# Performance work log

Hardware: AMD Instinct MI355X
Metric: run time of the kernel (lower is better)

## Reference

```python
import jax, jax.numpy as jnp
import numpy as np

D_MODEL = 2048
NUM_HEADS = 16
D_K = D_MODEL // NUM_HEADS
SEQ = 2048
BATCH = 2
THETA = 10000.0


def setup_inputs() -> dict:
    key = jax.random.key(0)
    ks = jax.random.split(key, 5)
    s = 1.0 / np.sqrt(D_MODEL)
    return {
        "x": jax.random.normal(ks[0], (BATCH, SEQ, D_MODEL), jnp.float32),
        "wq": jax.random.normal(ks[1], (D_MODEL, D_MODEL), jnp.float32) * s,
        "wk": jax.random.normal(ks[2], (D_MODEL, D_MODEL), jnp.float32) * s,
        "wv": jax.random.normal(ks[3], (D_MODEL, D_MODEL), jnp.float32) * s,
        "wo": jax.random.normal(ks[4], (D_MODEL, D_MODEL), jnp.float32) * s,
    }


def _rope_tables(seq_len, d_k, theta, dtype):
    pos = jnp.arange(seq_len, dtype=dtype)[:, None]            # [S,1]
    inv = theta ** (-(jnp.arange(0, d_k, 2, dtype=dtype) / d_k))  # [d_k/2]
    ang = pos * inv                                            # [S, d_k/2]
    sin = jnp.repeat(jnp.sin(ang), 2, axis=1)                  # [S, d_k] interleaved
    cos = jnp.repeat(jnp.cos(ang), 2, axis=1)
    return sin, cos


def _apply_rope(x, sin, cos):
    # x: [..., S, d_k]; interleaved-pair rotation
    xp = x.reshape(x.shape[:-1] + (x.shape[-1] // 2, 2))
    swapped = jnp.stack((-xp[..., 1], xp[..., 0]), axis=-1).reshape(x.shape)
    return x * cos + swapped * sin


def reference(x, wq, wk, wv, wo):
    B, S, D = x.shape
    H, dk = NUM_HEADS, D_K
    # projections: weights are (H*dk, D); q/k/v -> [B,H,S,dk]
    q = jnp.einsum("bsd,hkd->bhsk", x, wq.reshape(H, dk, D))
    k = jnp.einsum("bsd,hkd->bhsk", x, wk.reshape(H, dk, D))
    v = jnp.einsum("bsd,hkd->bhsk", x, wv.reshape(H, dk, D))
    sin, cos = _rope_tables(S, dk, THETA, x.dtype)
    q = _apply_rope(q, sin, cos)
    k = _apply_rope(k, sin, cos)
    scores = jnp.einsum("bhqk,bhsk->bhqs", q, k) / jnp.sqrt(jnp.asarray(dk, x.dtype))
    causal = jnp.triu(jnp.ones((S, S), dtype=bool), k=1)
    scores = jnp.where(causal, -jnp.inf, scores)
    attn = jax.nn.softmax(scores, axis=-1)
    out = jnp.einsum("bhqs,bhsv->bqhv", attn, v).reshape(B, S, H * dk)
    return jnp.einsum("bsf,df->bsd", out, wo)
```

## Files before the change

### kernel.cpp

```cpp
#include <hip/hip_runtime.h>
#include <hip/hip_bf16.h>

#define B_  2
#define S_  2048
#define D_  2048
#define H_  16
#define DK_ 128
#define M_  (B_*S_)

typedef unsigned short u16;
typedef short bf16x8 __attribute__((ext_vector_type(8)));
typedef float f32x4  __attribute__((ext_vector_type(4)));

#define NEG_BIG (-1.0e30f)

__device__ __forceinline__ u16 f2bf(float f){
    unsigned int u = __float_as_uint(f);
    unsigned int r = (u + 0x7fffu + ((u >> 16) & 1u)) >> 16;
    return (u16)r;
}

__device__ __forceinline__ uint4 cvt8(const float* p){
    float4 a = *(const float4*)p;
    float4 b = *(const float4*)(p + 4);
    uint4 r;
    r.x = ((unsigned int)f2bf(a.y) << 16) | (unsigned int)f2bf(a.x);
    r.y = ((unsigned int)f2bf(a.w) << 16) | (unsigned int)f2bf(a.z);
    r.z = ((unsigned int)f2bf(b.y) << 16) | (unsigned int)f2bf(b.x);
    r.w = ((unsigned int)f2bf(b.w) << 16) | (unsigned int)f2bf(b.z);
    return r;
}

__device__ __forceinline__ void unpack8(const uint4 v, float* f){
    f[0]=__uint_as_float(v.x<<16); f[1]=__uint_as_float(v.x&0xffff0000u);
    f[2]=__uint_as_float(v.y<<16); f[3]=__uint_as_float(v.y&0xffff0000u);
    f[4]=__uint_as_float(v.z<<16); f[5]=__uint_as_float(v.z&0xffff0000u);
    f[6]=__uint_as_float(v.w<<16); f[7]=__uint_as_float(v.w&0xffff0000u);
}

__device__ __forceinline__ void async16(const void* g, void* l){
    __builtin_amdgcn_global_load_lds(
        (const __attribute__((address_space(1))) void*)g,
        (__attribute__((address_space(3))) void*)l, 16, 0, 0);
}

__global__ __launch_bounds__(256) void cvt_all(
    const float* __restrict__ x,  const float* __restrict__ wq, const float* __restrict__ wk,
    const float* __restrict__ wv, const float* __restrict__ wo,
    u16* __restrict__ xb, u16* __restrict__ wqb, u16* __restrict__ wkb,
    u16* __restrict__ wvb, u16* __restrict__ wob)
{
    int c = blockIdx.x*256 + threadIdx.x;
    const float* src; u16* dst; int lc;
    if      (c < 1048576){ src = x;  dst = xb;  lc = c; }
    else if (c < 1572864){ src = wq; dst = wqb; lc = c - 1048576; }
    else if (c < 2097152){ src = wk; dst = wkb; lc = c - 1572864; }
    else if (c < 2621440){ src = wv; dst = wvb; lc = c - 2097152; }
    else                 { src = wo; dst = wob; lc = c - 2621440; }
    *(uint4*)&dst[(size_t)lc*8] = cvt8(&src[(size_t)lc*8]);
}

template<int MODE>
__global__ __launch_bounds__(512, 2) void gemm256(
    const u16* __restrict__ A, const u16* __restrict__ W0, const u16* __restrict__ W1,
    void* __restrict__ C0, void* __restrict__ C1)
{
    __shared__ __align__(16) u16 ring[4][2][8192];

    const int tid  = threadIdx.x;
    const int lane = tid & 63;
    const int w    = tid >> 6;
    const int quad = lane >> 4;
    const int l15  = lane & 15;
    const int wM   = w & 1;
    const int wN   = w >> 1;
    const int blockN = blockIdx.x * 256;
    const int blockM = blockIdx.y * 256;

    const u16* Wm; void* Cm;
    if (MODE == 0){ Wm = blockIdx.z ? W1 : W0; Cm = blockIdx.z ? (void*)C1 : (void*)C0; }
    else          { Wm = W0; Cm = C0; }

    const int cswz = quad ^ ((l15 >> 1) & 3);

    f32x4 acc[32];
    #pragma unroll
    for (int i = 0; i < 32; ++i) acc[i] = (f32x4){0.f,0.f,0.f,0.f};

    auto stage = [&](int t){
        const int k0 = t * 32;
        u16* la = (u16*)&ring[t & 3][0][0];
        u16* lb = (u16*)&ring[t & 3][1][0];
        #pragma unroll
        for (int it = 0; it < 2; ++it){
            int cc  = it*512 + tid;
            int row = cc >> 2;
            int g   = (cc & 3) ^ ((cc >> 3) & 3);
            int kb  = k0 + g*8;
            const u16* ga;
            if (MODE == 1){
                int rg = blockM + row;
                int b = rg >> 11, s2 = rg & 2047;
                int h = kb >> 7,  kk = kb & 127;
                ga = &A[(((size_t)(b*H_ + h))*S_ + s2)*DK_ + kk];
            } else {
                ga = &A[(size_t)(blockM + row)*2048 + kb];
            }
            async16(ga, la + cc*8);
            async16(&Wm[(size_t)(blockN + row)*2048 + kb], lb + cc*8);
        }
    };

    stage(0); stage(1); stage(2);
    asm volatile("s_waitcnt vmcnt(8)" ::: "memory");
    __builtin_amdgcn_s_barrier();
    __builtin_amdgcn_sched_barrier(0);

    for (int t = 0; t < 64; ++t){
        const u16* la = (const u16*)&ring[t & 3][0][0];
        const u16* lb = (const u16*)&ring[t & 3][1][0];

        if (t <= 60) stage(t + 3);

        bf16x8 bfv[4], af[4];
        #pragma unroll
        for (int ni = 0; ni < 4; ++ni)
            bfv[ni] = *(const bf16x8*)&lb[(wN*64 + ni*16 + l15)*32 + cswz*8];
        #pragma unroll
        for (int mi = 0; mi < 4; ++mi)
            af[mi]  = *(const bf16x8*)&la[(wM*128 + mi*16 + l15)*32 + cswz*8];

        __builtin_amdgcn_s_setprio(1);
        #pragma unroll
        for (int mi = 0; mi < 4; ++mi)
            #pragma unroll
            for (int ni = 0; ni < 4; ++ni)
                acc[mi*4+ni] = __builtin_amdgcn_mfma_f32_16x16x32_bf16(
                                   af[mi], bfv[ni], acc[mi*4+ni], 0, 0, 0);
        __builtin_amdgcn_s_setprio(0);

        #pragma unroll
        for (int mi = 0; mi < 4; ++mi)
            af[mi]  = *(const bf16x8*)&la[(wM*128 + 64 + mi*16 + l15)*32 + cswz*8];

        __builtin_amdgcn_s_setprio(1);
        #pragma unroll
        for (int mi = 0; mi < 4; ++mi)
            #pragma unroll
            for (int ni = 0; ni < 4; ++ni)
                acc[16 + mi*4+ni] = __builtin_amdgcn_mfma_f32_16x16x32_bf16(
                                   af[mi], bfv[ni], acc[16 + mi*4+ni], 0, 0, 0);
        __builtin_amdgcn_s_setprio(0);

        if (t <= 60)      { asm volatile("s_waitcnt vmcnt(8)" ::: "memory"); }
        else if (t == 61) { asm volatile("s_waitcnt vmcnt(4)" ::: "memory"); }
        else if (t == 62) { asm volatile("s_waitcnt vmcnt(0)" ::: "memory"); }
        __builtin_amdgcn_s_barrier();
        __builtin_amdgcn_sched_barrier(0);
    }

    #pragma unroll
    for (int hf = 0; hf < 2; ++hf){
        #pragma unroll
        for (int mi = 0; mi < 4; ++mi){
            #pragma unroll
            for (int ni = 0; ni < 4; ++ni){
                #pragma unroll
                for (int r = 0; r < 4; ++r){
                    float v = acc[hf*16 + mi*4+ni][r];
                    int row = blockM + wM*128 + hf*64 + mi*16 + quad*4 + r;
                    int col = blockN + wN*64 + ni*16 + l15;
                    if (MODE == 0){
                        int b = row >> 11, s2 = row & 2047;
                        int h = col >> 7,  kk = col & 127;
                        ((u16*)Cm)[(((size_t)(b*H_ + h))*S_ + s2)*DK_ + kk] = f2bf(v);
                    } else if (MODE == 2){
                        int h = row >> 7,  kk = row & 127;
                        int b = col >> 11, s2 = col & 2047;
                        ((u16*)Cm)[(((size_t)(b*H_ + h))*DK_ + kk)*S_ + s2] = f2bf(v);
                    } else {
                        ((float*)Cm)[(size_t)row*2048 + col] = v;
                    }
                }
            }
        }
    }
}

template<int MODE>
__global__ __launch_bounds__(256) void gemm_bt(
    const void* __restrict__ Av,
    const float* __restrict__ W0, const float* __restrict__ W1,
    void* __restrict__ C0, void* __restrict__ C1)
{
    __shared__ u16 As[128*40];
    __shared__ u16 Bs[128*40];

    const int tid  = threadIdx.x;
    const int lane = tid & 63;
    const int w    = tid >> 6;
    const int quad = lane >> 4;
    const int l15  = lane & 15;
    const int blockN = blockIdx.x * 128;
    const int blockM = blockIdx.y * 128;

    const float* Wm; void* Cm;
    if (MODE == 0){ Wm = blockIdx.z ? W1 : W0; Cm = blockIdx.z ? (void*)C1 : (void*)C0; }
    else          { Wm = W0; Cm = C0; }

    const int waveM = (w & 1) * 64;
    const int waveN = (w >> 1) * 64;

    f32x4 acc[16];
    #pragma unroll
    for (int i = 0; i < 16; ++i) acc[i] = (f32x4){0.f,0.f,0.f,0.f};

    for (int k0 = 0; k0 < 2048; k0 += 32){
        __syncthreads();
        #pragma unroll
        for (int it = 0; it < 2; ++it){
            int cc  = tid + it*256;
            int row = cc >> 2;
            int ch  = cc & 3;
            int kb  = k0 + ch*8;
            uint4 va;
            if (MODE == 1){
                int g = blockM + row;
                int b = g >> 11, s2 = g & 2047;
                int h = kb >> 7, kk = kb & 127;
                va = *(const uint4*)&((const u16*)Av)[(((size_t)(b*H_ + h))*S_ + s2)*DK_ + kk];
            } else {
                va = cvt8(&((const float*)Av)[(size_t)(blockM+row)*2048 + kb]);
            }
            uint4 vb = cvt8(&Wm[(size_t)(blockN+row)*2048 + kb]);
            *(uint4*)&As[row*40 + ch*8] = va;
            *(uint4*)&Bs[row*40 + ch*8] = vb;
        }
        __syncthreads();

        bf16x8 af[4], bfv[4];
        #pragma unroll
        for (int mi = 0; mi < 4; ++mi)
            af[mi]  = *(const bf16x8*)&As[(waveM + mi*16 + l15)*40 + quad*8];
        #pragma unroll
        for (int ni = 0; ni < 4; ++ni)
            bfv[ni] = *(const bf16x8*)&Bs[(waveN + ni*16 + l15)*40 + quad*8];
        #pragma unroll
        for (int mi = 0; mi < 4; ++mi)
            #pragma unroll
            for (int ni = 0; ni < 4; ++ni)
                acc[mi*4+ni] = __builtin_amdgcn_mfma_f32_16x16x32_bf16(
                                   af[mi], bfv[ni], acc[mi*4+ni], 0, 0, 0);
    }

    #pragma unroll
    for (int mi = 0; mi < 4; ++mi){
        #pragma unroll
        for (int ni = 0; ni < 4; ++ni){
            #pragma unroll
            for (int r = 0; r < 4; ++r){
                float v = acc[mi*4+ni][r];
                int row = blockM + waveM + mi*16 + quad*4 + r;
                int col = blockN + waveN + ni*16 + l15;
                if (MODE == 0){
                    int b = row >> 11, s2 = row & 2047;
                    int h = col >> 7,  kk = col & 127;
                    ((u16*)Cm)[(((size_t)(b*H_ + h))*S_ + s2)*DK_ + kk] = f2bf(v);
                } else if (MODE == 2){
                    int h = row >> 7,  kk = row & 127;
                    int b = col >> 11, s2 = col & 2047;
                    ((u16*)Cm)[(((size_t)(b*H_ + h))*DK_ + kk)*S_ + s2] = f2bf(v);
                } else {
                    ((float*)Cm)[(size_t)row*2048 + col] = v;
                }
            }
        }
    }
}

__global__ __launch_bounds__(256) void rope_kernel(u16* __restrict__ Q, u16* __restrict__ K)
{
    u16* T = blockIdx.y ? K : Q;
    const float osc = blockIdx.y ? 1.0f : 0.12751743f;
    int t  = blockIdx.x * 256 + threadIdx.x;
    int i0 = (t & 15) * 4;
    int s  = (t >> 4) & 2047;
    size_t base = ((size_t)(t >> 4)) * 128 + (size_t)i0 * 2;
    uint4 v = *(const uint4*)&T[base];
    float f[8]; unpack8(v, f);
    const float nl2t = -13.287712379549449f / 64.0f;
    float sf = (float)s;
    unsigned int out[4];
    #pragma unroll
    for (int p = 0; p < 4; ++p){
        float inv = exp2f((float)(i0 + p) * nl2t);
        float ang = sf * inv;
        float sn, cn;
        sincosf(ang, &sn, &cn);
        float e0 = f[2*p], e1 = f[2*p+1];
        float r0 = (e0*cn - e1*sn) * osc;
        float r1 = (e1*cn + e0*sn) * osc;
        out[p] = ((unsigned int)f2bf(r1) << 16) | (unsigned int)f2bf(r0);
    }
    uint4 ov; ov.x = out[0]; ov.y = out[1]; ov.z = out[2]; ov.w = out[3];
    *(uint4*)&T[base] = ov;
}

__global__ __launch_bounds__(256, 4) void attn_mfma(
    const u16* Q, const u16* __restrict__ K,
    const u16* __restrict__ VT, u16* O)
{
    __shared__ __align__(16) u16 Ks[64*128];
    __shared__ __align__(16) u16 Vs[128*64];
    __shared__ __align__(16) u16 Ps[4][16*64];

    const int tid  = threadIdx.x;
    const int bh   = blockIdx.x;
    const int qb   = (int)gridDim.y - 1 - (int)blockIdx.y;
    const int w    = tid >> 6;
    const int lane = tid & 63;
    const int quad = lane >> 4;
    const int l15  = lane & 15;
    const int sw   = l15 & 7;
    const size_t qkb = (size_t)bh * S_ * DK_;

    const int qw = qb*64 + w*16;

    bf16x8 aq[4];
    {
        const u16* qp = &Q[qkb + (size_t)(qw + l15)*128 + quad*8];
        #pragma unroll
        for (int kt = 0; kt < 4; ++kt)
            aq[kt] = *(const bf16x8*)(qp + kt*32);
    }

    f32x4 oa[8];
    #pragma unroll
    for (int vt = 0; vt < 8; ++vt) oa[vt] = (f32x4){0.f,0.f,0.f,0.f};
    float m_i = NEG_BIG, l_i = 0.f;

    const int nkb = qb + 1;
    for (int kb = 0; kb < nkb; ++kb){
        __syncthreads();
        #pragma unroll
        for (int it = 0; it < 4; ++it){
            int cc  = tid + it*256;
            int row = cc >> 4, cl = cc & 15;
            async16(&K[qkb + (size_t)(kb*64 + row)*128 + (size_t)((cl ^ (row & 7))*8)],
                    &Ks[cc*8]);
        }
        #pragma unroll
        for (int it = 0; it < 4; ++it){
            int cc  = tid + it*256;
            int row = cc >> 3, cl = cc & 7;
            async16(&VT[qkb + (size_t)row*S_ + (size_t)(kb*64 + (cl ^ (row & 7))*8)],
                    &Vs[cc*8]);
        }
        __syncthreads();

        if (kb*64 > qw + 15) continue;

        f32x4 s[4];
        __builtin_amdgcn_s_setprio(1);
        #pragma unroll
        for (int nt = 0; nt < 4; ++nt){
            f32x4 a = (f32x4){0.f,0.f,0.f,0.f};
            #pragma unroll
            for (int kt = 0; kt < 4; ++kt){
                bf16x8 ak = *(const bf16x8*)&Ks[(nt*16 + l15)*128 + ((kt*4 + quad) ^ sw)*8];
                a = __builtin_amdgcn_mfma_f32_16x16x32_bf16(ak, aq[kt], a, 0,0,0);
            }
            s[nt] = a;
        }
        __builtin_amdgcn_s_setprio(0);

        if (kb*64 + 63 > qw){
            int qg = qw + l15;
            #pragma unroll
            for (int nt = 0; nt < 4; ++nt)
                #pragma unroll
                for (int rr = 0; rr < 4; ++rr){
                    int jg = kb*64 + nt*16 + quad*4 + rr;
                    if (jg > qg) s[nt][rr] = NEG_BIG;
                }
        }

        float mx = s[0][0];
        #pragma unroll
        for (int nt = 0; nt < 4; ++nt)
            #pragma unroll
            for (int rr = 0; rr < 4; ++rr) mx = fmaxf(mx, s[nt][rr]);
        mx = fmaxf(mx, __shfl_xor(mx, 16, 64));
        mx = fmaxf(mx, __shfl_xor(mx, 32, 64));

        if (!__all((mx - m_i) <= 8.0f)){
            float mn = fmaxf(m_i, mx);
            float al = exp2f(m_i - mn);
            m_i = mn;
            l_i *= al;
            float al4[4];
            #pragma unroll
            for (int rr = 0; rr < 4; ++rr)
                al4[rr] = __shfl(al, (lane & 48) | (quad*4 + rr), 64);
            #pragma unroll
            for (int vt = 0; vt < 8; ++vt)
                #pragma unroll
                for (int rr = 0; rr < 4; ++rr) oa[vt][rr] *= al4[rr];
        }

        float ps = 0.f;
        #pragma unroll
        for (int nt = 0; nt < 4; ++nt)
            #pragma unroll
            for (int rr = 0; rr < 4; ++rr){
                float p = exp2f(s[nt][rr] - m_i);
                s[nt][rr] = p; ps += p;
            }
        ps += __shfl_xor(ps, 16, 64);
        ps += __shfl_xor(ps, 32, 64);
        l_i += ps;

        u16* pw = Ps[w];
        #pragma unroll
        for (int nt = 0; nt < 4; ++nt){
            uint2 pk;
            asm("v_cvt_pk_bf16_f32 %0, %1, %2" : "=v"(pk.x) : "v"(s[nt][0]), "v"(s[nt][1]));
            asm("v_cvt_pk_bf16_f32 %0, %1, %2" : "=v"(pk.y) : "v"(s[nt][2]), "v"(s[nt][3]));
            int c = (nt*2 + (quad >> 1)) ^ sw;
            *(uint2*)&pw[l15*64 + c*8 + (quad & 1)*4] = pk;
        }

        bf16x8 pa[2];
        #pragma unroll
        for (int kt = 0; kt < 2; ++kt)
            pa[kt] = *(const bf16x8*)&pw[l15*64 + ((kt*4 + quad) ^ sw)*8];

        __builtin_amdgcn_s_setprio(1);
        #pragma unroll
        for (int vt = 0; vt < 8; ++vt){
            #pragma unroll
            for (int kt = 0; kt < 2; ++kt){
                bf16x8 bv = *(const bf16x8*)&Vs[(vt*16 + l15)*64 + ((kt*4 + quad) ^ sw)*8];
                oa[vt] = __builtin_amdgcn_mfma_f32_16x16x32_bf16(pa[kt], bv, oa[vt], 0,0,0);
            }
        }
        __builtin_amdgcn_s_setprio(0);
    }

    #pragma unroll
    for (int rr = 0; rr < 4; ++rr){
        float lv = __shfl(l_i, (lane & 48) | (quad*4 + rr), 64);
        float inv = 1.f / lv;
        int qg = qw + quad*4 + rr;
        #pragma unroll
        for (int vt = 0; vt < 8; ++vt)
            O[qkb + (size_t)qg*128 + vt*16 + l15] = f2bf(oa[vt][rr] * inv);
    }
}

extern "C" void kernel_launch(void* const* d_in, const int* in_sizes, int n_in,
                              void* d_out, int out_size, void* d_ws, size_t ws_size,
                              hipStream_t stream)
{
    const float* x  = (const float*)d_in[0];
    const float* wq = (const float*)d_in[1];
    const float* wk = (const float*)d_in[2];
    const float* wv = (const float*)d_in[3];
    const float* wo = (const float*)d_in[4];
    float* out = (float*)d_out;

    const size_t NT = (size_t)B_ * H_ * S_ * DK_;
    const size_t NW = (size_t)D_ * D_;

    if (ws_size >= (size_t)50331648){
        u16* Qw  = (u16*)d_ws;
        u16* Kw  = Qw + NT;
        u16* wvb = Qw + 2*NT;
        u16* wob = wvb + NW;
        u16* xb  = (u16*)d_out;
        u16* wqb = xb + NT;
        u16* wkb = wqb + NW;
        u16* VT  = xb + NT;
        u16* Ow  = Qw;

        cvt_all<<<dim3(12288), 256, 0, stream>>>(x, wq, wk, wv, wo,
                                                 xb, wqb, wkb, wvb, wob);
        gemm256<0><<<dim3(8, 16, 2), 512, 0, stream>>>(xb, wqb, wkb, Qw, Kw);
        gemm256<2><<<dim3(16, 8, 1), 512, 0, stream>>>(wvb, xb, nullptr, VT, nullptr);
        rope_kernel<<<dim3(4096, 2), 256, 0, stream>>>(Qw, Kw);
        attn_mfma<<<dim3(32, 32), 256, 0, stream>>>(Qw, Kw, VT, Ow);
        gemm256<1><<<dim3(8, 16, 1), 512, 0, stream>>>(Ow, wob, nullptr, out, nullptr);
    } else {
        u16* Qw  = (u16*)d_ws;
        u16* Vtd = (u16*)d_out;
        u16* Kw  = (u16*)d_out + NT;
        u16* Ow  = Qw;
        gemm_bt<0><<<dim3(16, 32, 2), 256, 0, stream>>>(x, wq, wk, Qw, Kw);
        gemm_bt<2><<<dim3(32, 16, 1), 256, 0, stream>>>(wv, x, nullptr, Vtd, nullptr);
        rope_kernel<<<dim3(4096, 2), 256, 0, stream>>>(Qw, Kw);
        attn_mfma<<<dim3(32, 32), 256, 0, stream>>>(Qw, Kw, Vtd, Ow);
        gemm_bt<1><<<dim3(16, 32, 1), 256, 0, stream>>>(Ow, wo, nullptr, out, nullptr);
    }
}
```

Baseline: 396.1 us.

## Process two 16-row query tiles per warp in attention kernel

```diff
diff --git a/kernel.cpp b/kernel.cpp
--- a/kernel.cpp
+++ b/kernel.cpp
@@ -306,13 +306,13 @@
     *(uint4*)&T[base] = ov;
 }
 
-__global__ __launch_bounds__(256, 4) void attn_mfma(
+__global__ __launch_bounds__(256, 3) void attn_mfma(
     const u16* Q, const u16* __restrict__ K,
     const u16* __restrict__ VT, u16* O)
 {
     __shared__ __align__(16) u16 Ks[64*128];
     __shared__ __align__(16) u16 Vs[128*64];
-    __shared__ __align__(16) u16 Ps[4][16*64];
+    __shared__ __align__(16) u16 Ps[4][32*64];
 
     const int tid  = threadIdx.x;
     const int bh   = blockIdx.x;
@@ -324,22 +324,27 @@
     const int sw   = l15 & 7;
     const size_t qkb = (size_t)bh * S_ * DK_;
 
-    const int qw = qb*64 + w*16;
-
-    bf16x8 aq[4];
-    {
-        const u16* qp = &Q[qkb + (size_t)(qw + l15)*128 + quad*8];
+    const int qw = qb*128 + w*32;
+
+    bf16x8 aq[2][4];
+    #pragma unroll
+    for (int mt = 0; mt < 2; ++mt){
+        const u16* qp = &Q[qkb + (size_t)(qw + mt*16 + l15)*128 + quad*8];
         #pragma unroll
         for (int kt = 0; kt < 4; ++kt)
-            aq[kt] = *(const bf16x8*)(qp + kt*32);
-    }
-
-    f32x4 oa[8];
-    #pragma unroll
-    for (int vt = 0; vt < 8; ++vt) oa[vt] = (f32x4){0.f,0.f,0.f,0.f};
-    float m_i = NEG_BIG, l_i = 0.f;
-
-    const int nkb = qb + 1;
+            aq[mt][kt] = *(const bf16x8*)(qp + kt*32);
+    }
+
+    f32x4 oa[2][8];
+    float m_i[2], l_i[2];
+    #pragma unroll
+    for (int mt = 0; mt < 2; ++mt){
+        #pragma unroll
+        for (int vt = 0; vt < 8; ++vt) oa[mt][vt] = (f32x4){0.f,0.f,0.f,0.f};
+        m_i[mt] = NEG_BIG; l_i[mt] = 0.f;
+    }
+
+    const int nkb = 2*qb + 2;
     for (int kb = 0; kb < nkb; ++kb){
         __syncthreads();
         #pragma unroll
@@ -358,103 +363,126 @@
         }
         __syncthreads();
 
-        if (kb*64 > qw + 15) continue;
-
-        f32x4 s[4];
+        if (kb*64 > qw + 31) continue;
+
+        f32x4 s[2][4];
         __builtin_amdgcn_s_setprio(1);
         #pragma unroll
         for (int nt = 0; nt < 4; ++nt){
-            f32x4 a = (f32x4){0.f,0.f,0.f,0.f};
-            #pragma unroll
-            for (int kt = 0; kt < 4; ++kt){
-                bf16x8 ak = *(const bf16x8*)&Ks[(nt*16 + l15)*128 + ((kt*4 + quad) ^ sw)*8];
-                a = __builtin_amdgcn_mfma_f32_16x16x32_bf16(ak, aq[kt], a, 0,0,0);
-            }
-            s[nt] = a;
+            bf16x8 ak[4];
+            #pragma unroll
+            for (int kt = 0; kt < 4; ++kt)
+                ak[kt] = *(const bf16x8*)&Ks[(nt*16 + l15)*128 + ((kt*4 + quad) ^ sw)*8];
+            #pragma unroll
+            for (int mt = 0; mt < 2; ++mt){
+                f32x4 a = (f32x4){0.f,0.f,0.f,0.f};
+                #pragma unroll
+                for (int kt = 0; kt < 4; ++kt)
+                    a = __builtin_amdgcn_mfma_f32_16x16x32_bf16(ak[kt], aq[mt][kt], a, 0,0,0);
+                s[mt][nt] = a;
+            }
         }
         __builtin_amdgcn_s_setprio(0);
 
         if (kb*64 + 63 > qw){
-            int qg = qw + l15;
+            #pragma unroll
+            for (int mt = 0; mt < 2; ++mt){
+                int qg = qw + mt*16 + l15;
+                #pragma unroll
+                for (int nt = 0; nt < 4; ++nt)
+                    #pragma unroll
+                    for (int rr = 0; rr < 4; ++rr){
+                        int jg = kb*64 + nt*16 + quad*4 + rr;
+                        if (jg > qg) s[mt][nt][rr] = NEG_BIG;
+                    }
+            }
+        }
+
+        #pragma unroll
+        for (int mt = 0; mt < 2; ++mt){
+            float mx = s[mt][0][0];
             #pragma unroll
             for (int nt = 0; nt < 4; ++nt)
                 #pragma unroll
+                for (int rr = 0; rr < 4; ++rr) mx = fmaxf(mx, s[mt][nt][rr]);
+            mx = fmaxf(mx, __shfl_xor(mx, 16, 64));
+            mx = fmaxf(mx, __shfl_xor(mx, 32, 64));
+
+            if (!__all((mx - m_i[mt]) <= 8.0f)){
+                float mn = fmaxf(m_i[mt], mx);
+                float al = exp2f(m_i[mt] - mn);
+                m_i[mt] = mn;
+                l_i[mt] *= al;
+                float al4[4];
+                #pragma unroll
+                for (int rr = 0; rr < 4; ++rr)
+                    al4[rr] = __shfl(al, (lane & 48) | (quad*4 + rr), 64);
+                #pragma unroll
+                for (int vt = 0; vt < 8; ++vt)
+                    #pragma unroll
+                    for (int rr = 0; rr < 4; ++rr) oa[mt][vt][rr] *= al4[rr];
+            }
+
+            float ps = 0.f;
+            #pragma unroll
+            for (int nt = 0; nt < 4; ++nt)
+                #pragma unroll
                 for (int rr = 0; rr < 4; ++rr){
-                    int jg = kb*64 + nt*16 + quad*4 + rr;
-                    if (jg > qg) s[nt][rr] = NEG_BIG;
+                    float p = exp2f(s[mt][nt][rr] - m_i[mt]);
+                    s[mt][nt][rr] = p; ps += p;
                 }
-        }
-
-        float mx = s[0][0];
-        #pragma unroll
-        for (int nt = 0; nt < 4; ++nt)
-            #pragma unroll
-            for (int rr = 0; rr < 4; ++rr) mx = fmaxf(mx, s[nt][rr]);
-        mx = fmaxf(mx, __shfl_xor(mx, 16, 64));
-        mx = fmaxf(mx, __shfl_xor(mx, 32, 64));
-
-        if (!__all((mx - m_i) <= 8.0f)){
-            float mn = fmaxf(m_i, mx);
-            float al = exp2f(m_i - mn);
-            m_i = mn;
-            l_i *= al;
-            float al4[4];
-            #pragma unroll
-            for (int rr = 0; rr < 4; ++rr)
-                al4[rr] = __shfl(al, (lane & 48) | (quad*4 + rr), 64);
+            ps += __shfl_xor(ps, 16, 64);
+            ps += __shfl_xor(ps, 32, 64);
+            l_i[mt] += ps;
+        }
+
+        u16* pw = Ps[w];
+        #pragma unroll
+        for (int mt = 0; mt < 2; ++mt)
+          #pragma unroll
+          for (int nt = 0; nt < 4; ++nt){
+              uint2 pk;
+              asm("v_cvt_pk_bf16_f32 %0, %1, %2" : "=v"(pk.x) : "v"(s[mt][nt][0]), "v"(s[mt][nt][1]));
+              asm("v_cvt_pk_bf16_f32 %0, %1, %2" : "=v"(pk.y) : "v"(s[mt][nt][2]), "v"(s[mt][nt][3]));
+              int c = (nt*2 + (quad >> 1)) ^ sw;
+              *(uint2*)&pw[(mt*16 + l15)*64 + c*8 + (quad & 1)*4] = pk;
+          }
+
+        bf16x8 pa[2][2];
+        #pragma unroll
+        for (int mt = 0; mt < 2; ++mt)
+          #pragma unroll
+          for (int kt = 0; kt < 2; ++kt)
+            pa[mt][kt] = *(const bf16x8*)&pw[(mt*16 + l15)*64 + ((kt*4 + quad) ^ sw)*8];
+
+        __builtin_amdgcn_s_setprio(1);
+        #pragma unroll
+        for (int vt = 0; vt < 8; ++vt){
+            bf16x8 bv[2];
+            #pragma unroll
+            for (int kt = 0; kt < 2; ++kt)
+                bv[kt] = *(const bf16x8*)&Vs[(vt*16 + l15)*64 + ((kt*4 + quad) ^ sw)*8];
+            #pragma unroll
+            for (int mt = 0; mt < 2; ++mt)
+              #pragma unroll
+              for (int kt = 0; kt < 2; ++kt)
+                oa[mt][vt] = __builtin_amdgcn_mfma_f32_16x16x32_bf16(
+                                 pa[mt][kt], bv[kt], oa[mt][vt], 0,0,0);
+        }
+        __builtin_amdgcn_s_setprio(0);
+    }
+
+    #pragma unroll
+    for (int mt = 0; mt < 2; ++mt){
+        #pragma unroll
+        for (int rr = 0; rr < 4; ++rr){
+            float lv = __shfl(l_i[mt], (lane & 48) | (quad*4 + rr), 64);
+            float inv = 1.f / lv;
+            int qg = qw + mt*16 + quad*4 + rr;
             #pragma unroll
             for (int vt = 0; vt < 8; ++vt)
-                #pragma unroll
-                for (int rr = 0; rr < 4; ++rr) oa[vt][rr] *= al4[rr];
-        }
-
-        float ps = 0.f;
-        #pragma unroll
-        for (int nt = 0; nt < 4; ++nt)
-            #pragma unroll
-            for (int rr = 0; rr < 4; ++rr){
-                float p = exp2f(s[nt][rr] - m_i);
-                s[nt][rr] = p; ps += p;
-            }
-        ps += __shfl_xor(ps, 16, 64);
-        ps += __shfl_xor(ps, 32, 64);
-        l_i += ps;
-
-        u16* pw = Ps[w];
-        #pragma unroll
-        for (int nt = 0; nt < 4; ++nt){
-            uint2 pk;
-            asm("v_cvt_pk_bf16_f32 %0, %1, %2" : "=v"(pk.x) : "v"(s[nt][0]), "v"(s[nt][1]));
-            asm("v_cvt_pk_bf16_f32 %0, %1, %2" : "=v"(pk.y) : "v"(s[nt][2]), "v"(s[nt][3]));
-            int c = (nt*2 + (quad >> 1)) ^ sw;
-            *(uint2*)&pw[l15*64 + c*8 + (quad & 1)*4] = pk;
-        }
-
-        bf16x8 pa[2];
-        #pragma unroll
-        for (int kt = 0; kt < 2; ++kt)
-            pa[kt] = *(const bf16x8*)&pw[l15*64 + ((kt*4 + quad) ^ sw)*8];
-
-        __builtin_amdgcn_s_setprio(1);
-        #pragma unroll
-        for (int vt = 0; vt < 8; ++vt){
-            #pragma unroll
-            for (int kt = 0; kt < 2; ++kt){
-                bf16x8 bv = *(const bf16x8*)&Vs[(vt*16 + l15)*64 + ((kt*4 + quad) ^ sw)*8];
-                oa[vt] = __builtin_amdgcn_mfma_f32_16x16x32_bf16(pa[kt], bv, oa[vt], 0,0,0);
-            }
-        }
-        __builtin_amdgcn_s_setprio(0);
-    }
-
-    #pragma unroll
-    for (int rr = 0; rr < 4; ++rr){
-        float lv = __shfl(l_i, (lane & 48) | (quad*4 + rr), 64);
-        float inv = 1.f / lv;
-        int qg = qw + quad*4 + rr;
-        #pragma unroll
-        for (int vt = 0; vt < 8; ++vt)
-            O[qkb + (size_t)qg*128 + vt*16 + l15] = f2bf(oa[vt][rr] * inv);
+                O[qkb + (size_t)qg*128 + vt*16 + l15] = f2bf(oa[mt][vt][rr] * inv);
+        }
     }
 }
 
@@ -488,7 +516,7 @@
         gemm256<0><<<dim3(8, 16, 2), 512, 0, stream>>>(xb, wqb, wkb, Qw, Kw);
         gemm256<2><<<dim3(16, 8, 1), 512, 0, stream>>>(wvb, xb, nullptr, VT, nullptr);
         rope_kernel<<<dim3(4096, 2), 256, 0, stream>>>(Qw, Kw);
-        attn_mfma<<<dim3(32, 32), 256, 0, stream>>>(Qw, Kw, VT, Ow);
+        attn_mfma<<<dim3(32, 16), 256, 0, stream>>>(Qw, Kw, VT, Ow);
         gemm256<1><<<dim3(8, 16, 1), 512, 0, stream>>>(Ow, wob, nullptr, out, nullptr);
     } else {
         u16* Qw  = (u16*)d_ws;
@@ -498,7 +526,7 @@
         gemm_bt<0><<<dim3(16, 32, 2), 256, 0, stream>>>(x, wq, wk, Qw, Kw);
         gemm_bt<2><<<dim3(32, 16, 1), 256, 0, stream>>>(wv, x, nullptr, Vtd, nullptr);
         rope_kernel<<<dim3(4096, 2), 256, 0, stream>>>(Qw, Kw);
-        attn_mfma<<<dim3(32, 32), 256, 0, stream>>>(Qw, Kw, Vtd, Ow);
+        attn_mfma<<<dim3(32, 16), 256, 0, stream>>>(Qw, Kw, Vtd, Ow);
         gemm_bt<1><<<dim3(16, 32, 1), 256, 0, stream>>>(Ow, wo, nullptr, out, nullptr);
     }
 }
```

Result: slower. 431.3 us (+8.9%).
